# Kernel tuning notes

Measured on AMD Instinct MI355X. Metric: run time of the kernel, lower is better.

Reference implementation:

```python
import itertools
import jax, jax.numpy as jnp
import numpy as np

CUTOFF = 5.0
N_IMAGES = 1
MAX_PAIRS = 262144  # static upper bound on close pairs (expected ~65K)
BOX = 16.0
EPS = 1e-5


def setup_inputs() -> dict:
    key = jax.random.key(0)
    n_mol, n_atoms = 32, 128
    coordinates = jax.random.uniform(key, (n_mol, n_atoms, 3), dtype=jnp.float32) * BOX
    nonblank = jnp.ones((n_mol, n_atoms), dtype=bool)
    real_atoms = jnp.arange(n_mol * n_atoms, dtype=jnp.int32)
    inv_real_atoms = jnp.arange(n_mol * n_atoms, dtype=jnp.int32)
    cells = jnp.tile((jnp.eye(3, dtype=jnp.float32) * BOX)[None], (n_mol, 1, 1))
    combinator = jnp.asarray(
        np.array(list(itertools.product(range(-N_IMAGES, N_IMAGES + 1), repeat=3)), dtype=np.float32)
    )
    return {
        "coordinates": coordinates,
        "nonblank": nonblank,
        "real_atoms": real_atoms,
        "inv_real_atoms": inv_real_atoms,
        "cells": cells,
        "combinator": combinator,
    }


def reference(coordinates, nonblank, real_atoms, inv_real_atoms, cells, combinator):
    n_mol, n_atoms, _ = coordinates.shape
    flat_pairs = n_mol * n_atoms * n_atoms

    atom_index = jnp.arange(n_mol * n_atoms, dtype=jnp.int32).reshape(n_mol, n_atoms)
    nonblank_pair = (nonblank[:, :, None] & nonblank[:, None, :]).reshape(flat_pairs)

    pair_first_all = jnp.broadcast_to(atom_index[:, :, None], (n_mol, n_atoms, n_atoms)).reshape(flat_pairs)
    pair_second_all = jnp.broadcast_to(atom_index[:, None, :], (n_mol, n_atoms, n_atoms)).reshape(flat_pairs)
    mol_of_pair = jnp.broadcast_to(
        jnp.arange(n_mol, dtype=jnp.int32)[:, None, None], (n_mol, n_atoms, n_atoms)
    ).reshape(flat_pairs)

    # pair_diffcoords[p] = r_i - r_j for pair p (row-major over b, a1, a2)
    diff = (coordinates[:, :, None, :] - coordinates[:, None, :, :]).reshape(flat_pairs, 3)

    # cell_shifts[o, b, d] = sum_c combinator[o, c] * cells[b, c, d]
    cell_shifts = jnp.einsum("oc,bcd->obd", combinator, cells)
    offsets = cell_shifts[:, mol_of_pair]  # (n_off, flat_pairs, 3)

    pair_dist = jnp.linalg.norm(diff[None] + offsets, axis=2)  # (n_off, flat_pairs)
    close = (pair_dist < CUTOFF) & (pair_dist > EPS) & nonblank_pair[None]

    # static-size nonzero; jnp.nonzero returns row-major sorted indices, so the
    # first n_valid slots are exactly torch.nonzero's output, rest are padding.
    cp_offset, cp_pair = jnp.nonzero(close, size=MAX_PAIRS, fill_value=0)
    n_valid = jnp.sum(close)
    valid = jnp.arange(MAX_PAIRS) < n_valid

    pair_first = jnp.where(valid, inv_real_atoms[pair_first_all[cp_pair]], 0)
    pair_second = jnp.where(valid, inv_real_atoms[pair_second_all[cp_pair]], 0)
    pair_offsets = jnp.where(valid[:, None], offsets[cp_offset, cp_pair], 0.0)
    cell_offsets = jnp.where(valid[:, None], combinator[cp_offset], 0.0)
    cp_offset = jnp.where(valid, cp_offset, 0)

    coordflat = coordinates.reshape(n_mol * n_atoms, 3)[real_atoms]
    paircoord = (coordflat[pair_first] - coordflat[pair_second] + pair_offsets) * valid[:, None]
    sq = jnp.sum(paircoord * paircoord, axis=1)
    distflat2 = jnp.sqrt(jnp.where(sq > 0, sq, 1.0)) * (sq > 0)

    return distflat2, pair_first, pair_second, paircoord, cell_offsets, cp_offset
```

## Files before the change

### kernel.cpp

```cpp
#include <hip/hip_runtime.h>
#include <stdint.h>

#define N_OFF 27
#define FLAT_PAIRS (32 * 128 * 128)
#define MAX_PAIRS 262144
#define GRAN_P 2048
#define PBLK 256
#define NGRAN (N_OFF * PBLK)
#define WPG 32
#define NWORDS (N_OFF * (FLAT_PAIRS / 64))
#define CUTOFF_F 5.0f
#define EPS_F 1e-5f


__global__ __launch_bounds__(256) void ppi_mask(
    const float* __restrict__ coords,
    unsigned long long* __restrict__ words,
    uint32_t* __restrict__ blkcnt) {
    const int blk = blockIdx.x;
    const int tid = threadIdx.x;
    const int lane = tid & 63;
    const int wave = tid >> 6;
    __shared__ unsigned long long lw[N_OFF * WPG];
    for (int k = tid; k < N_OFF * WPG; k += 256) lw[k] = 0;
    __syncthreads();

    const int pbase = blk * GRAN_P;
    #pragma unroll
    for (int r = 0; r < GRAN_P / 256; ++r) {
        const int p = pbase + r * 256 + tid;
        const int ai = p >> 7;
        const int aj = ((p >> 14) << 7) | (p & 127);
        const float* ci = coords + ai * 3;
        const float* cj = coords + aj * 3;
        const float dx0 = ci[0] - cj[0];
        const float dy0 = ci[1] - cj[1];
        const float dz0 = ci[2] - cj[2];
        const int ox = (dx0 > 8.f) ? -1 : (dx0 < -8.f) ? 1 : 0;
        const int oy = (dy0 > 8.f) ? -1 : (dy0 < -8.f) ? 1 : 0;
        const int oz = (dz0 > 8.f) ? -1 : (dz0 < -8.f) ? 1 : 0;
        const float dx = dx0 + 16.f * (float)ox;
        const float dy = dy0 + 16.f * (float)oy;
        const float dz = dz0 + 16.f * (float)oz;
        const float xx = dx * dx;
        const float yy = dy * dy;
        const float zz = dz * dz;
        const float s1 = xx + yy;
        const float sq = s1 + zz;
        const float dist = sqrtf(sq);
        const bool close = (dist < CUTOFF_F) && (dist > EPS_F);
        const int o = 9 * ox + 3 * oy + oz + 13;

        const int chunk = r * 4 + wave;
        unsigned long long active = __ballot(close);
        while (active) {
            const int src = (int)__builtin_ctzll(active);
            const int oo = __shfl(o, src);
            const unsigned long long grp = __ballot(close && (o == oo));
            if (lane == src) lw[oo * WPG + chunk] = grp;
            active &= ~grp;
        }
    }
    __syncthreads();

    for (int idx = tid; idx < N_OFF * WPG; idx += 256) {
        const int o_ = idx >> 5;
        const int c = idx & 31;
        const unsigned long long w = lw[idx];
        words[(o_ << 13) + (blk << 5) + c] = w;
        uint32_t pc = (uint32_t)__popcll(w);
        #pragma unroll
        for (int d = 16; d; d >>= 1) pc += __shfl_xor(pc, d);
        if (c == 0) blkcnt[o_ * PBLK + blk] = pc;
    }
}

__global__ __launch_bounds__(1024) void ppi_gather(
    const float* __restrict__ coords,
    const int* __restrict__ inv_real,
    const unsigned long long* __restrict__ words,
    const uint32_t* __restrict__ blkcnt,
    float* __restrict__ out) {
    const int tid = threadIdx.x;

    __shared__ uint32_t lc[NGRAN];
    __shared__ uint32_t bpre[257];
    __shared__ uint32_t sh[256];

    for (int k = tid; k < NGRAN; k += 1024) lc[k] = blkcnt[k];
    __syncthreads();
    uint32_t s = 0;
    if (tid < 256) {
        const int cb = tid * 27;
        #pragma unroll
        for (int k = 0; k < 27; ++k) s += lc[cb + k];
        sh[tid] = s;
    }
    __syncthreads();
    #pragma unroll
    for (int d = 1; d < 256; d <<= 1) {
        uint32_t v = 0;
        if (tid < 256 && tid >= d) v = sh[tid - d];
        __syncthreads();
        if (tid < 256) sh[tid] += v;
        __syncthreads();
    }
    if (tid < 256) bpre[tid] = sh[tid] - s;
    if (tid == 255) bpre[256] = sh[255];
    __syncthreads();
    const uint32_t nv = bpre[256];

    const int q = blockIdx.x * 1024 + tid;
    float dist = 0.f, f0 = 0.f, f1 = 0.f, f2 = 0.f;
    float dx = 0.f, dy = 0.f, dz = 0.f, pf = 0.f, ps = 0.f, fo = 0.f;

    if ((uint32_t)q < nv) {
        int lo = 0, hi = 256;
        while (hi - lo > 1) {
            const int mid = (lo + hi) >> 1;
            if (bpre[mid] <= (uint32_t)q) lo = mid; else hi = mid;
        }
        uint32_t rr = (uint32_t)q - bpre[lo];
        int g = lo * 27;
        while (rr >= lc[g]) { rr -= lc[g]; ++g; }
        const unsigned long long* wbase = words + ((size_t)g << 5);
        const unsigned long long* wp = wbase;
        unsigned long long w = *wp;
        int r2 = (int)rr;
        for (;;) {
            const int pc = (int)__popcll(w);
            if (r2 < pc) break;
            r2 -= pc;
            w = *++wp;
        }
        for (int k = 0; k < r2; ++k) w &= w - 1ull;
        const int bit = (int)__builtin_ctzll(w);
        const int c = (int)(wp - wbase);
        const int o = g >> 8;
        const int p = ((g & 255) << 11) + (c << 6) + bit;
        const int ai = p >> 7;
        const int aj = ((p >> 14) << 7) | (p & 127);
        const int oa = o / 9;
        const int obt = (o - 9 * oa) / 3;
        const int ocv = o - 9 * oa - 3 * obt;
        f0 = (float)(oa - 1); f1 = (float)(obt - 1); f2 = (float)(ocv - 1);
        const float sx = 16.f * f0, sy = 16.f * f1, sz = 16.f * f2;
        const float* ci = coords + ai * 3;
        const float* cj = coords + aj * 3;
        dx = ci[0] - cj[0] + sx;
        dy = ci[1] - cj[1] + sy;
        dz = ci[2] - cj[2] + sz;
        const float xx = dx * dx;
        const float yy = dy * dy;
        const float zz = dz * dz;
        const float s1 = xx + yy;
        const float sq = s1 + zz;
        dist = sqrtf(sq);
        pf = (float)inv_real[ai];
        ps = (float)inv_real[aj];
        fo = (float)o;
    }

    out[q] = dist;
    out[MAX_PAIRS + q] = pf;
    out[2 * MAX_PAIRS + q] = ps;
    float* pcd = out + 3 * MAX_PAIRS + 3 * q;
    pcd[0] = dx; pcd[1] = dy; pcd[2] = dz;
    float* cod = out + 6 * MAX_PAIRS + 3 * q;
    cod[0] = f0; cod[1] = f1; cod[2] = f2;
    out[9 * MAX_PAIRS + q] = fo;
}

extern "C" void kernel_launch(void* const* d_in, const int* in_sizes, int n_in,
                              void* d_out, int out_size, void* d_ws, size_t ws_size,
                              hipStream_t stream) {
    (void)in_sizes; (void)n_in; (void)out_size; (void)ws_size;
    const float* coords = (const float*)d_in[0];
    const int* inv_real = (const int*)d_in[3];
    float* out = (float*)d_out;

    unsigned long long* words = (unsigned long long*)d_ws;
    uint32_t* blkcnt = (uint32_t*)((char*)d_ws + (size_t)NWORDS * 8);

    ppi_mask<<<PBLK, 256, 0, stream>>>(coords, words, blkcnt);
    ppi_gather<<<MAX_PAIRS / 1024, 1024, 0, stream>>>(coords, inv_real, words,
                                                      blkcnt, out);
}
```

Baseline: 26.54 us.

## Replace linear rank scans in gather with per-word prefix sums and binary search

The mask kernel now stores a 16-bit exclusive prefix count for every 64-bit mask word, built with a wave-level shfl_up scan, alongside the per-granule totals. The gather kernel turns each 27-entry group of granule counts into an inclusive prefix in shared memory. Each output slot then finds its granule and its word by binary search, and the target bit by a popcount bisection, instead of the earlier linear loops over counts, words and bits. This removes long, divergent per-thread scans, at the cost of extra workspace, extra global writes in the mask kernel and one more dependent global load per thread.

```diff
diff --git a/kernel.cpp b/kernel.cpp
--- a/kernel.cpp
+++ b/kernel.cpp
@@ -16,6 +16,7 @@
 __global__ __launch_bounds__(256) void ppi_mask(
     const float* __restrict__ coords,
     unsigned long long* __restrict__ words,
+    uint16_t* __restrict__ wpre,
     uint32_t* __restrict__ blkcnt) {
     const int blk = blockIdx.x;
     const int tid = threadIdx.x;
@@ -67,11 +68,17 @@
         const int o_ = idx >> 5;
         const int c = idx & 31;
         const unsigned long long w = lw[idx];
-        words[(o_ << 13) + (blk << 5) + c] = w;
-        uint32_t pc = (uint32_t)__popcll(w);
-        #pragma unroll
-        for (int d = 16; d; d >>= 1) pc += __shfl_xor(pc, d);
-        if (c == 0) blkcnt[o_ * PBLK + blk] = pc;
+        const int g = o_ * PBLK + blk;
+        words[((size_t)g << 5) + c] = w;
+        const uint32_t pc = (uint32_t)__popcll(w);
+        uint32_t incl = pc;
+        #pragma unroll
+        for (int d = 1; d < 32; d <<= 1) {
+            const uint32_t v = __shfl_up(incl, d, 32);
+            if (c >= d) incl += v;
+        }
+        wpre[((size_t)g << 5) + c] = (uint16_t)(incl - pc);
+        if (c == 31) blkcnt[g] = incl;
     }
 }
 
@@ -79,6 +86,7 @@
     const float* __restrict__ coords,
     const int* __restrict__ inv_real,
     const unsigned long long* __restrict__ words,
+    const uint16_t* __restrict__ wpre,
     const uint32_t* __restrict__ blkcnt,
     float* __restrict__ out) {
     const int tid = threadIdx.x;
@@ -93,7 +101,7 @@
     if (tid < 256) {
         const int cb = tid * 27;
         #pragma unroll
-        for (int k = 0; k < 27; ++k) s += lc[cb + k];
+        for (int k = 0; k < 27; ++k) { s += lc[cb + k]; lc[cb + k] = s; }
         sh[tid] = s;
     }
     __syncthreads();
@@ -105,7 +113,12 @@
         if (tid < 256) sh[tid] += v;
         __syncthreads();
     }
-    if (tid < 256) bpre[tid] = sh[tid] - s;
+    if (tid < 256) bpre[tid] = sh[tid] - ((tid < 256) ? (sh[tid] - (bpre[0], sh[tid])) : 0);
+    __syncthreads();
+    if (tid < 256) {
+        uint32_t total_k = (tid == 0) ? 0u : sh[tid - 1];
+        bpre[tid] = total_k;
+    }
     if (tid == 255) bpre[256] = sh[255];
     __syncthreads();
     const uint32_t nv = bpre[256];
@@ -120,22 +133,43 @@
             const int mid = (lo + hi) >> 1;
             if (bpre[mid] <= (uint32_t)q) lo = mid; else hi = mid;
         }
-        uint32_t rr = (uint32_t)q - bpre[lo];
-        int g = lo * 27;
-        while (rr >= lc[g]) { rr -= lc[g]; ++g; }
-        const unsigned long long* wbase = words + ((size_t)g << 5);
-        const unsigned long long* wp = wbase;
-        unsigned long long w = *wp;
-        int r2 = (int)rr;
-        for (;;) {
-            const int pc = (int)__popcll(w);
-            if (r2 < pc) break;
-            r2 -= pc;
-            w = *++wp;
-        }
-        for (int k = 0; k < r2; ++k) w &= w - 1ull;
-        const int bit = (int)__builtin_ctzll(w);
-        const int c = (int)(wp - wbase);
+        const uint32_t rr = (uint32_t)q - bpre[lo];
+        const int cb = lo * 27;
+        int k = 0;
+        #pragma unroll
+        for (int step = 16; step; step >>= 1) {
+            const int nk = k + step;
+            if (nk <= 27 && lc[cb + nk - 1] <= rr) k = nk;
+        }
+        const int g = cb + k;
+        uint32_t r2 = rr - (k ? lc[cb + k - 1] : 0u);
+        const uint16_t* wp16 = wpre + ((size_t)g << 5);
+        int c = 0;
+        #pragma unroll
+        for (int step = 16; step; step >>= 1) {
+            const int nc = c + step;
+            if (nc < 32 && (uint32_t)wp16[nc] <= r2) c = nc;
+        }
+        r2 -= (uint32_t)wp16[c];
+        const unsigned long long w = words[((size_t)g << 5) + c];
+        int pos = 0;
+        uint32_t x = (uint32_t)w;
+        {
+            const uint32_t cl = (uint32_t)__popc(x);
+            if (r2 >= cl) { r2 -= cl; pos = 32; x = (uint32_t)(w >> 32); }
+        }
+        uint32_t ch = (uint32_t)__popc(x & 0xFFFFu);
+        if (r2 >= ch) { r2 -= ch; pos += 16; x >>= 16; }
+        ch = (uint32_t)__popc(x & 0xFFu);
+        if (r2 >= ch) { r2 -= ch; pos += 8; x >>= 8; }
+        ch = (uint32_t)__popc(x & 0xFu);
+        if (r2 >= ch) { r2 -= ch; pos += 4; x >>= 4; }
+        ch = (uint32_t)__popc(x & 0x3u);
+        if (r2 >= ch) { r2 -= ch; pos += 2; x >>= 2; }
+        ch = x & 1u;
+        if (r2 >= ch) { pos += 1; }
+        const int bit = pos;
+
         const int o = g >> 8;
         const int p = ((g & 255) << 11) + (c << 6) + bit;
         const int ai = p >> 7;
@@ -180,9 +214,10 @@
     float* out = (float*)d_out;
 
     unsigned long long* words = (unsigned long long*)d_ws;
-    uint32_t* blkcnt = (uint32_t*)((char*)d_ws + (size_t)NWORDS * 8);
-
-    ppi_mask<<<PBLK, 256, 0, stream>>>(coords, words, blkcnt);
+    uint16_t* wpre = (uint16_t*)((char*)d_ws + (size_t)NWORDS * 8);
+    uint32_t* blkcnt = (uint32_t*)((char*)d_ws + (size_t)NWORDS * 8 + (size_t)NWORDS * 2);
+
+    ppi_mask<<<PBLK, 256, 0, stream>>>(coords, words, wpre, blkcnt);
     ppi_gather<<<MAX_PAIRS / 1024, 1024, 0, stream>>>(coords, inv_real, words,
-                                                      blkcnt, out);
+                                                      wpre, blkcnt, out);
 }
```

Measured after the change: 21.93 us. 17.4% less time.
